# Kernel tuning notes

Hardware: AMD Instinct MI355X
Metric: run time of the kernel (lower is better)

## Reference

```python
import jax, jax.numpy as jnp
import numpy as np

N_NODES = 2048


def setup_inputs() -> dict:
    key = jax.random.key(0)
    ks = jax.random.split(key, 9)
    N, IN, HID, OUT, R, B1 = N_NODES, 64, 32, 16, 4, 1
    s = 0.1
    return {
        "x": jax.random.normal(ks[0], (N, IN), jnp.float32),
        # adj_initial = ones - eye, as in __init__ (learnable parameter)
        "adj_matrix": jnp.ones((N, N), jnp.float32) - jnp.eye(N, dtype=jnp.float32),
        "bases1": jax.random.normal(ks[1], (B1, IN, HID), jnp.float32) * s,
        "coeff1": jax.random.normal(ks[2], (R, B1), jnp.float32) * s,
        "loop_w1": jax.random.normal(ks[3], (IN, HID), jnp.float32) * s,
        "bias1": jnp.zeros((HID,), jnp.float32),
        "bases2": jax.random.normal(ks[4], (R, HID, OUT), jnp.float32) * s,
        "coeff2": jax.random.normal(ks[5], (R, R), jnp.float32) * s,
        "loop_w2": jax.random.normal(ks[6], (HID, OUT), jnp.float32) * s,
        "bias2": jnp.zeros((OUT,), jnp.float32),
        "edge_type": 0,  # ignored by the module (etype is rebuilt as zeros)
    }


def _rel_graph_conv(h, bases, coeff, loop_w, bias, src, dst, n_nodes, act):
    # basis regularizer: W_r = sum_b coeff[r, b] * bases[b]; all edges have etype 0
    W0 = jnp.einsum('b,bio->io', coeff[0], bases)          # [in, out]
    msg = (h @ W0)[src]                                    # [E, out] gather-by-edge
    agg = jax.ops.segment_sum(msg, dst, num_segments=n_nodes)  # scatter-sum
    out = agg + h @ loop_w + bias                          # self-loop + bias
    return act(out)


def reference(x, adj_matrix, bases1, coeff1, loop_w1, bias1,
              bases2, coeff2, loop_w2, bias2, edge_type):
    N = x.shape[0]
    # sigmoid(adj_matrix) > 0 everywhere (sigmoid(0)=0.5 on the diagonal), so
    # torch.nonzero yields ALL N^2 pairs in row-major order: complete graph
    # with self-loops. Structure is static -> build edges with arange.
    idx = jnp.arange(N)
    src = jnp.repeat(idx, N)   # [N*N]
    dst = jnp.tile(idx, N)     # [N*N]
    h = _rel_graph_conv(x, bases1, coeff1, loop_w1, bias1, src, dst, N, jax.nn.relu)
    h = _rel_graph_conv(h, bases2, coeff2, loop_w2, bias2, src, dst, N, lambda z: z)
    return h
```

## Files before the change

### kernel.cpp

```cpp
#include <hip/hip_runtime.h>

#define NN   2048
#define IN   64
#define HID  32
#define OUTD 16

#define S0P 0
#define H1O 4096
#define S1P (4096 + NN * HID)

__global__ __launch_bounds__(256) void k1_colsum_x(const float* __restrict__ x,
                                                   float* __restrict__ ws) {
    __shared__ float red[256];
    const int tid = threadIdx.x, b = blockIdx.x;
    const int col = tid & 63, grp = tid >> 6;
    const float* xb = x + b * 32 * IN;
    float s = 0.f;
#pragma unroll
    for (int r = 0; r < 8; ++r)
        s += xb[(grp * 8 + r) * IN + col];
    red[tid] = s;
    __syncthreads();
    if (tid < 64)
        ws[S0P + b * 64 + tid] = red[tid] + red[tid + 64] + red[tid + 128] + red[tid + 192];
}

__global__ __launch_bounds__(256) void k2_layer1(const float* __restrict__ x,
                                                 const float* __restrict__ bases1,
                                                 const float* __restrict__ coeff1,
                                                 const float* __restrict__ loop_w1,
                                                 const float* __restrict__ bias1,
                                                 float* __restrict__ ws) {
    __shared__ float w1sh[IN * HID];
    __shared__ float xsh[32 * IN];
    __shared__ float s0sh[IN];
    __shared__ float agg1sh[HID];
    __shared__ float red[256];
    const int tid = threadIdx.x, b = blockIdx.x;

    const float4* x4  = (const float4*)(x + b * 32 * IN);
    const float4* w14 = (const float4*)loop_w1;
    float4 xa = x4[tid], xb4 = x4[tid + 256];
    float4 wa = w14[tid], wb = w14[tid + 256];

    {
        const int col = tid & 63, g = tid >> 6;
        float a0 = 0.f, a1 = 0.f, a2 = 0.f, a3 = 0.f;
#pragma unroll
        for (int k = 0; k < 4; ++k) {
            a0 += ws[S0P + (g * 16 + k     ) * 64 + col];
            a1 += ws[S0P + (g * 16 + 4 + k ) * 64 + col];
            a2 += ws[S0P + (g * 16 + 8 + k ) * 64 + col];
            a3 += ws[S0P + (g * 16 + 12 + k) * 64 + col];
        }
        ((float4*)xsh)[tid] = xa; ((float4*)xsh)[tid + 256] = xb4;
        ((float4*)w1sh)[tid] = wa; ((float4*)w1sh)[tid + 256] = wb;
        red[tid] = a0 + a1 + a2 + a3;
    }
    __syncthreads();
    if (tid < 64)
        s0sh[tid] = red[tid] + red[tid + 64] + red[tid + 128] + red[tid + 192];
    __syncthreads();

    {
        const int h = tid & 31, seg = tid >> 5;
        float p = 0.f;
#pragma unroll
        for (int k = 0; k < 8; ++k)
            p += s0sh[seg * 8 + k] * bases1[(seg * 8 + k) * HID + h];
        red[tid] = p;
        __syncthreads();
        if (tid < HID) {
            float t = 0.f;
#pragma unroll
            for (int g = 0; g < 8; ++g) t += red[g * 32 + tid];
            agg1sh[tid] = bias1[tid] + coeff1[0] * t;
        }
    }
    __syncthreads();

    {
        const int h = tid & 31, rgrp = tid >> 5;
        const float agg1v = agg1sh[h];
        float a0 = agg1v, a1 = agg1v, a2 = agg1v, a3 = agg1v;
#pragma unroll
        for (int k = 0; k < IN; ++k) {
            const float w = w1sh[k * HID + h];
            a0 += xsh[(rgrp +  0) * IN + k] * w;
            a1 += xsh[(rgrp +  8) * IN + k] * w;
            a2 += xsh[(rgrp + 16) * IN + k] * w;
            a3 += xsh[(rgrp + 24) * IN + k] * w;
        }
        a0 = fmaxf(a0, 0.f); a1 = fmaxf(a1, 0.f);
        a2 = fmaxf(a2, 0.f); a3 = fmaxf(a3, 0.f);
        float* h1b = ws + H1O + b * 32 * HID;
        h1b[(rgrp +  0) * HID + h] = a0;
        h1b[(rgrp +  8) * HID + h] = a1;
        h1b[(rgrp + 16) * HID + h] = a2;
        h1b[(rgrp + 24) * HID + h] = a3;
        red[tid] = a0 + a1 + a2 + a3;
    }
    __syncthreads();
    if (tid < HID) {
        float t = 0.f;
#pragma unroll
        for (int g = 0; g < 8; ++g) t += red[g * 32 + tid];
        ws[S1P + b * HID + tid] = t;
    }
}

__global__ __launch_bounds__(256) void k3_layer2(const float* __restrict__ bases2,
                                                 const float* __restrict__ coeff2,
                                                 const float* __restrict__ loop_w2,
                                                 const float* __restrict__ bias2,
                                                 const float* __restrict__ ws,
                                                 float* __restrict__ out) {
    __shared__ float w2sh[HID * OUTD];
    __shared__ float w2csh[HID * OUTD];
    __shared__ float h1sh[16 * (HID + 1)];
    __shared__ float s1sh[HID];
    __shared__ float agg2sh[OUTD];
    __shared__ float red[256];
    const int tid = threadIdx.x, b = blockIdx.x;

    {
        const float c20 = coeff2[0], c21 = coeff2[1], c22 = coeff2[2], c23 = coeff2[3];
#pragma unroll
        for (int j = 0; j < 2; ++j) {
            const int i = tid + j * 256;
            w2sh[i]  = loop_w2[i];
            w2csh[i] = c20 * bases2[i]        + c21 * bases2[512 + i] +
                       c22 * bases2[1024 + i] + c23 * bases2[1536 + i];
        }
    }
    for (int j = 0; j < 2; ++j) {
        const int i = tid + j * 256;
        h1sh[(i >> 5) * (HID + 1) + (i & 31)] = ws[H1O + b * 16 * HID + i];
    }
    {
        const int h = tid & 31, g = tid >> 5;
        float a0 = 0.f, a1 = 0.f;
#pragma unroll
        for (int k = 0; k < 4; ++k) {
            a0 += ws[S1P + (g * 8 + k    ) * HID + h];
            a1 += ws[S1P + (g * 8 + 4 + k) * HID + h];
        }
        red[tid] = a0 + a1;
    }
    __syncthreads();
    if (tid < HID) {
        float t = 0.f;
#pragma unroll
        for (int g = 0; g < 8; ++g) t += red[g * 32 + tid];
        s1sh[tid] = t;
    }
    __syncthreads();
    if (tid < OUTD) {
        float s = 0.f;
#pragma unroll
        for (int h = 0; h < HID; ++h) s += s1sh[h] * w2csh[h * OUTD + tid];
        agg2sh[tid] = bias2[tid] + s;
    }
    __syncthreads();

    {
        const int row = tid >> 4, o = tid & 15;
        float acc = agg2sh[o];
#pragma unroll
        for (int h = 0; h < HID; ++h)
            acc += h1sh[row * (HID + 1) + h] * w2sh[h * OUTD + o];
        out[b * 256 + tid] = acc;
    }
}

extern "C" void kernel_launch(void* const* d_in, const int* in_sizes, int n_in,
                              void* d_out, int out_size, void* d_ws, size_t ws_size,
                              hipStream_t stream) {
    const float* x       = (const float*)d_in[0];
    const float* bases1  = (const float*)d_in[2];
    const float* coeff1  = (const float*)d_in[3];
    const float* loop_w1 = (const float*)d_in[4];
    const float* bias1   = (const float*)d_in[5];
    const float* bases2  = (const float*)d_in[6];
    const float* coeff2  = (const float*)d_in[7];
    const float* loop_w2 = (const float*)d_in[8];
    const float* bias2   = (const float*)d_in[9];
    float* out = (float*)d_out;
    float* ws  = (float*)d_ws;

    k1_colsum_x<<<64, 256, 0, stream>>>(x, ws);
    k2_layer1 <<<64, 256, 0, stream>>>(x, bases1, coeff1, loop_w1, bias1, ws);
    k3_layer2 <<<128, 256, 0, stream>>>(bases2, coeff2, loop_w2, bias2, ws, out);
}
```

Measured before the change: 89.29 us.

## Fuse three kernels into one persistent kernel with flag-based grid barriers

Merges the column-sum, layer-1 and layer-2 kernels into a single 64-block launch. Cross-block reductions are synchronised with magic-value release/acquire flags in workspace instead of kernel boundaries. Layer-1 activations stay in shared memory rather than going through global memory. This removes two launch gaps and the h1 global round-trip. In exchange it relies on all 64 blocks being co-resident and on spin barriers with a guard timeout. Flags are never reset, so stale values from a previous call could satisfy the barrier early.

```diff
diff --git a/kernel.cpp b/kernel.cpp
--- a/kernel.cpp
+++ b/kernel.cpp
@@ -4,58 +4,93 @@
 #define IN   64
 #define HID  32
 #define OUTD 16
+#define NB   64
+#define MAGICA 0x5CA1AB1Eu
+#define MAGICB 0x00DDBA11u
 
 #define S0P 0
-#define H1O 4096
-#define S1P (4096 + NN * HID)
-
-__global__ __launch_bounds__(256) void k1_colsum_x(const float* __restrict__ x,
-                                                   float* __restrict__ ws) {
+#define FLA 4096
+#define S1P 4160
+#define FLB 6208
+
+__global__ __launch_bounds__(256) void rgcn_1node(
+    const float* __restrict__ x,
+    const float* __restrict__ bases1,
+    const float* __restrict__ coeff1,
+    const float* __restrict__ loop_w1,
+    const float* __restrict__ bias1,
+    const float* __restrict__ bases2,
+    const float* __restrict__ coeff2,
+    const float* __restrict__ loop_w2,
+    const float* __restrict__ bias2,
+    float* __restrict__ ws,
+    float* __restrict__ out)
+{
+    __shared__ float xsh[32 * IN];
+    __shared__ float w1sh[IN * HID];
+    __shared__ float w2sh[HID * OUTD];
+    __shared__ float w2csh[HID * OUTD];
+    __shared__ float h1sh[32 * (HID + 1)];
     __shared__ float red[256];
-    const int tid = threadIdx.x, b = blockIdx.x;
-    const int col = tid & 63, grp = tid >> 6;
-    const float* xb = x + b * 32 * IN;
-    float s = 0.f;
-#pragma unroll
-    for (int r = 0; r < 8; ++r)
-        s += xb[(grp * 8 + r) * IN + col];
-    red[tid] = s;
-    __syncthreads();
-    if (tid < 64)
-        ws[S0P + b * 64 + tid] = red[tid] + red[tid + 64] + red[tid + 128] + red[tid + 192];
-}
-
-__global__ __launch_bounds__(256) void k2_layer1(const float* __restrict__ x,
-                                                 const float* __restrict__ bases1,
-                                                 const float* __restrict__ coeff1,
-                                                 const float* __restrict__ loop_w1,
-                                                 const float* __restrict__ bias1,
-                                                 float* __restrict__ ws) {
-    __shared__ float w1sh[IN * HID];
-    __shared__ float xsh[32 * IN];
     __shared__ float s0sh[IN];
     __shared__ float agg1sh[HID];
-    __shared__ float red[256];
+    __shared__ float s1sh[HID];
+    __shared__ float agg2sh[OUTD];
+
     const int tid = threadIdx.x, b = blockIdx.x;
+    unsigned int* flagsA = (unsigned int*)ws + FLA;
+    unsigned int* flagsB = (unsigned int*)ws + FLB;
 
     const float4* x4  = (const float4*)(x + b * 32 * IN);
     const float4* w14 = (const float4*)loop_w1;
-    float4 xa = x4[tid], xb4 = x4[tid + 256];
+    float4 xa = x4[tid], xb = x4[tid + 256];
     float4 wa = w14[tid], wb = w14[tid + 256];
+    const float c20 = coeff2[0], c21 = coeff2[1], c22 = coeff2[2], c23 = coeff2[3];
+    float w2v0 = loop_w2[tid], w2v1 = loop_w2[tid + 256];
+    float wc0 = c20 * bases2[tid]       + c21 * bases2[512 + tid] +
+                c22 * bases2[1024 + tid]+ c23 * bases2[1536 + tid];
+    float wc1 = c20 * bases2[256 + tid] + c21 * bases2[768 + tid] +
+                c22 * bases2[1280 + tid]+ c23 * bases2[1792 + tid];
+    ((float4*)xsh)[tid] = xa;  ((float4*)xsh)[tid + 256] = xb;
+    ((float4*)w1sh)[tid] = wa; ((float4*)w1sh)[tid + 256] = wb;
+    w2sh[tid] = w2v0;  w2sh[tid + 256] = w2v1;
+    w2csh[tid] = wc0;  w2csh[tid + 256] = wc1;
+    __syncthreads();
+
+    {
+        const int col = tid & 63, grp = tid >> 6;
+        float s = 0.f;
+#pragma unroll
+        for (int r = 0; r < 8; ++r) s += xsh[(grp * 8 + r) * IN + col];
+        red[tid] = s;
+    }
+    __syncthreads();
+    if (tid < 64) {
+        float v = red[tid] + red[tid + 64] + red[tid + 128] + red[tid + 192];
+        __hip_atomic_store(&ws[S0P + b * 64 + tid], v,
+                           __ATOMIC_RELAXED, __HIP_MEMORY_SCOPE_AGENT);
+    }
+    __syncthreads();
+    if (tid == 0)
+        __hip_atomic_store(&flagsA[b], MAGICA,
+                           __ATOMIC_RELEASE, __HIP_MEMORY_SCOPE_AGENT);
+    if (tid < 64) {
+        int guard = 0; unsigned v;
+        do {
+            v = __hip_atomic_load(&flagsA[tid],
+                                  __ATOMIC_ACQUIRE, __HIP_MEMORY_SCOPE_AGENT);
+        } while (v != MAGICA && ++guard < 4000000);
+    }
+    __syncthreads();
 
     {
         const int col = tid & 63, g = tid >> 6;
-        float a0 = 0.f, a1 = 0.f, a2 = 0.f, a3 = 0.f;
-#pragma unroll
-        for (int k = 0; k < 4; ++k) {
-            a0 += ws[S0P + (g * 16 + k     ) * 64 + col];
-            a1 += ws[S0P + (g * 16 + 4 + k ) * 64 + col];
-            a2 += ws[S0P + (g * 16 + 8 + k ) * 64 + col];
-            a3 += ws[S0P + (g * 16 + 12 + k) * 64 + col];
-        }
-        ((float4*)xsh)[tid] = xa; ((float4*)xsh)[tid + 256] = xb4;
-        ((float4*)w1sh)[tid] = wa; ((float4*)w1sh)[tid + 256] = wb;
-        red[tid] = a0 + a1 + a2 + a3;
+        float s = 0.f;
+#pragma unroll
+        for (int k = 0; k < 16; ++k)
+            s += __hip_atomic_load(&ws[S0P + (g * 16 + k) * 64 + col],
+                                   __ATOMIC_RELAXED, __HIP_MEMORY_SCOPE_AGENT);
+        red[tid] = s;
     }
     __syncthreads();
     if (tid < 64)
@@ -69,20 +104,20 @@
         for (int k = 0; k < 8; ++k)
             p += s0sh[seg * 8 + k] * bases1[(seg * 8 + k) * HID + h];
         red[tid] = p;
-        __syncthreads();
-        if (tid < HID) {
-            float t = 0.f;
-#pragma unroll
-            for (int g = 0; g < 8; ++g) t += red[g * 32 + tid];
-            agg1sh[tid] = bias1[tid] + coeff1[0] * t;
-        }
+    }
+    __syncthreads();
+    if (tid < HID) {
+        float t = 0.f;
+#pragma unroll
+        for (int g = 0; g < 8; ++g) t += red[g * 32 + tid];
+        agg1sh[tid] = bias1[tid] + coeff1[0] * t;
     }
     __syncthreads();
 
     {
         const int h = tid & 31, rgrp = tid >> 5;
-        const float agg1v = agg1sh[h];
-        float a0 = agg1v, a1 = agg1v, a2 = agg1v, a3 = agg1v;
+        const float A = agg1sh[h];
+        float a0 = A, a1 = A, a2 = A, a3 = A;
 #pragma unroll
         for (int k = 0; k < IN; ++k) {
             const float w = w1sh[k * HID + h];
@@ -93,11 +128,10 @@
         }
         a0 = fmaxf(a0, 0.f); a1 = fmaxf(a1, 0.f);
         a2 = fmaxf(a2, 0.f); a3 = fmaxf(a3, 0.f);
-        float* h1b = ws + H1O + b * 32 * HID;
-        h1b[(rgrp +  0) * HID + h] = a0;
-        h1b[(rgrp +  8) * HID + h] = a1;
-        h1b[(rgrp + 16) * HID + h] = a2;
-        h1b[(rgrp + 24) * HID + h] = a3;
+        h1sh[(rgrp +  0) * (HID + 1) + h] = a0;
+        h1sh[(rgrp +  8) * (HID + 1) + h] = a1;
+        h1sh[(rgrp + 16) * (HID + 1) + h] = a2;
+        h1sh[(rgrp + 24) * (HID + 1) + h] = a3;
         red[tid] = a0 + a1 + a2 + a3;
     }
     __syncthreads();
@@ -105,47 +139,30 @@
         float t = 0.f;
 #pragma unroll
         for (int g = 0; g < 8; ++g) t += red[g * 32 + tid];
-        ws[S1P + b * HID + tid] = t;
-    }
-}
-
-__global__ __launch_bounds__(256) void k3_layer2(const float* __restrict__ bases2,
-                                                 const float* __restrict__ coeff2,
-                                                 const float* __restrict__ loop_w2,
-                                                 const float* __restrict__ bias2,
-                                                 const float* __restrict__ ws,
-                                                 float* __restrict__ out) {
-    __shared__ float w2sh[HID * OUTD];
-    __shared__ float w2csh[HID * OUTD];
-    __shared__ float h1sh[16 * (HID + 1)];
-    __shared__ float s1sh[HID];
-    __shared__ float agg2sh[OUTD];
-    __shared__ float red[256];
-    const int tid = threadIdx.x, b = blockIdx.x;
-
-    {
-        const float c20 = coeff2[0], c21 = coeff2[1], c22 = coeff2[2], c23 = coeff2[3];
-#pragma unroll
-        for (int j = 0; j < 2; ++j) {
-            const int i = tid + j * 256;
-            w2sh[i]  = loop_w2[i];
-            w2csh[i] = c20 * bases2[i]        + c21 * bases2[512 + i] +
-                       c22 * bases2[1024 + i] + c23 * bases2[1536 + i];
-        }
-    }
-    for (int j = 0; j < 2; ++j) {
-        const int i = tid + j * 256;
-        h1sh[(i >> 5) * (HID + 1) + (i & 31)] = ws[H1O + b * 16 * HID + i];
-    }
+        __hip_atomic_store(&ws[S1P + b * HID + tid], t,
+                           __ATOMIC_RELAXED, __HIP_MEMORY_SCOPE_AGENT);
+    }
+    __syncthreads();
+    if (tid == 0)
+        __hip_atomic_store(&flagsB[b], MAGICB,
+                           __ATOMIC_RELEASE, __HIP_MEMORY_SCOPE_AGENT);
+    if (tid < 64) {
+        int guard = 0; unsigned v;
+        do {
+            v = __hip_atomic_load(&flagsB[tid],
+                                  __ATOMIC_ACQUIRE, __HIP_MEMORY_SCOPE_AGENT);
+        } while (v != MAGICB && ++guard < 4000000);
+    }
+    __syncthreads();
+
     {
         const int h = tid & 31, g = tid >> 5;
-        float a0 = 0.f, a1 = 0.f;
-#pragma unroll
-        for (int k = 0; k < 4; ++k) {
-            a0 += ws[S1P + (g * 8 + k    ) * HID + h];
-            a1 += ws[S1P + (g * 8 + 4 + k) * HID + h];
-        }
-        red[tid] = a0 + a1;
+        float s = 0.f;
+#pragma unroll
+        for (int k = 0; k < 8; ++k)
+            s += __hip_atomic_load(&ws[S1P + (g * 8 + k) * HID + h],
+                                   __ATOMIC_RELAXED, __HIP_MEMORY_SCOPE_AGENT);
+        red[tid] = s;
     }
     __syncthreads();
     if (tid < HID) {
@@ -163,13 +180,15 @@
     }
     __syncthreads();
 
-    {
-        const int row = tid >> 4, o = tid & 15;
+#pragma unroll
+    for (int j = 0; j < 2; ++j) {
+        const int idx = tid + j * 256;
+        const int row = idx >> 4, o = idx & 15;
         float acc = agg2sh[o];
 #pragma unroll
         for (int h = 0; h < HID; ++h)
             acc += h1sh[row * (HID + 1) + h] * w2sh[h * OUTD + o];
-        out[b * 256 + tid] = acc;
+        out[b * 512 + idx] = acc;
     }
 }
 
@@ -188,7 +207,6 @@
     float* out = (float*)d_out;
     float* ws  = (float*)d_ws;
 
-    k1_colsum_x<<<64, 256, 0, stream>>>(x, ws);
-    k2_layer1 <<<64, 256, 0, stream>>>(x, bases1, coeff1, loop_w1, bias1, ws);
-    k3_layer2 <<<128, 256, 0, stream>>>(bases2, coeff2, loop_w2, bias2, ws, out);
+    rgcn_1node<<<NB, 256, 0, stream>>>(x, bases1, coeff1, loop_w1, bias1,
+                                       bases2, coeff2, loop_w2, bias2, ws, out);
 }
```

After: 93.17 us. +4.3%, slower.

## Fuse x column-sum into layer-1 kernel, each block recomputing the full reduction

Applied to the files above, without the earlier changes.

Removes the separate column-sum kernel. Every layer-1 block now reads all of x (512 KB) itself with float4 loads and reduces it to the 64 column sums, instead of reading per-block partials from workspace. This saves one kernel launch and the global round-trip between kernels. In exchange, the reads of x grow 64-fold in total (mostly served from L2) and each block carries 16 float4 accumulators in registers.

```diff
diff --git a/kernel.cpp b/kernel.cpp
--- a/kernel.cpp
+++ b/kernel.cpp
@@ -5,61 +5,59 @@
 #define HID  32
 #define OUTD 16
 
-#define S0P 0
-#define H1O 4096
-#define S1P (4096 + NN * HID)
+#define H1O 0
+#define S1P (NN * HID)
 
-__global__ __launch_bounds__(256) void k1_colsum_x(const float* __restrict__ x,
-                                                   float* __restrict__ ws) {
-    __shared__ float red[256];
-    const int tid = threadIdx.x, b = blockIdx.x;
-    const int col = tid & 63, grp = tid >> 6;
-    const float* xb = x + b * 32 * IN;
-    float s = 0.f;
-#pragma unroll
-    for (int r = 0; r < 8; ++r)
-        s += xb[(grp * 8 + r) * IN + col];
-    red[tid] = s;
-    __syncthreads();
-    if (tid < 64)
-        ws[S0P + b * 64 + tid] = red[tid] + red[tid + 64] + red[tid + 128] + red[tid + 192];
-}
-
-__global__ __launch_bounds__(256) void k2_layer1(const float* __restrict__ x,
+__global__ __launch_bounds__(256) void kA_layer1(const float* __restrict__ x,
                                                  const float* __restrict__ bases1,
                                                  const float* __restrict__ coeff1,
                                                  const float* __restrict__ loop_w1,
                                                  const float* __restrict__ bias1,
                                                  float* __restrict__ ws) {
+    __shared__ float xsh[32 * IN];
     __shared__ float w1sh[IN * HID];
-    __shared__ float xsh[32 * IN];
+    __shared__ float red4[1024];
     __shared__ float s0sh[IN];
     __shared__ float agg1sh[HID];
     __shared__ float red[256];
     const int tid = threadIdx.x, b = blockIdx.x;
 
-    const float4* x4  = (const float4*)(x + b * 32 * IN);
+    const float4* xt4 = (const float4*)(x + b * 32 * IN);
     const float4* w14 = (const float4*)loop_w1;
-    float4 xa = x4[tid], xb4 = x4[tid + 256];
+    float4 xa = xt4[tid], xb = xt4[tid + 256];
     float4 wa = w14[tid], wb = w14[tid + 256];
 
     {
-        const int col = tid & 63, g = tid >> 6;
-        float a0 = 0.f, a1 = 0.f, a2 = 0.f, a3 = 0.f;
+        const float4* x4 = (const float4*)x;
+        float4 acc[16];
 #pragma unroll
-        for (int k = 0; k < 4; ++k) {
-            a0 += ws[S0P + (g * 16 + k     ) * 64 + col];
-            a1 += ws[S0P + (g * 16 + 4 + k ) * 64 + col];
-            a2 += ws[S0P + (g * 16 + 8 + k ) * 64 + col];
-            a3 += ws[S0P + (g * 16 + 12 + k) * 64 + col];
+        for (int k = 0; k < 16; ++k) acc[k] = make_float4(0.f, 0.f, 0.f, 0.f);
+#pragma unroll
+        for (int ol = 0; ol < 8; ++ol) {
+#pragma unroll
+            for (int k = 0; k < 16; ++k) {
+                const float4 v = x4[ol * 4096 + k * 256 + tid];
+                acc[k].x += v.x; acc[k].y += v.y; acc[k].z += v.z; acc[k].w += v.w;
+            }
         }
-        ((float4*)xsh)[tid] = xa; ((float4*)xsh)[tid + 256] = xb4;
+#pragma unroll
+        for (int k = 1; k < 16; ++k) {
+            acc[0].x += acc[k].x; acc[0].y += acc[k].y;
+            acc[0].z += acc[k].z; acc[0].w += acc[k].w;
+        }
+        ((float4*)red4)[tid] = acc[0];
+        ((float4*)xsh)[tid] = xa;  ((float4*)xsh)[tid + 256] = xb;
         ((float4*)w1sh)[tid] = wa; ((float4*)w1sh)[tid + 256] = wb;
-        red[tid] = a0 + a1 + a2 + a3;
     }
     __syncthreads();
-    if (tid < 64)
-        s0sh[tid] = red[tid] + red[tid + 64] + red[tid + 128] + red[tid + 192];
+    if (tid < IN) {
+        const int cg = tid >> 2, comp = tid & 3;
+        float s = 0.f;
+#pragma unroll
+        for (int j = 0; j < 16; ++j)
+            s += red4[(cg + 16 * j) * 4 + comp];
+        s0sh[tid] = s;
+    }
     __syncthreads();
 
     {
@@ -69,20 +67,20 @@
         for (int k = 0; k < 8; ++k)
             p += s0sh[seg * 8 + k] * bases1[(seg * 8 + k) * HID + h];
         red[tid] = p;
-        __syncthreads();
-        if (tid < HID) {
-            float t = 0.f;
+    }
+    __syncthreads();
+    if (tid < HID) {
+        float t = 0.f;
 #pragma unroll
-            for (int g = 0; g < 8; ++g) t += red[g * 32 + tid];
-            agg1sh[tid] = bias1[tid] + coeff1[0] * t;
-        }
+        for (int g = 0; g < 8; ++g) t += red[g * 32 + tid];
+        agg1sh[tid] = bias1[tid] + coeff1[0] * t;
     }
     __syncthreads();
 
     {
         const int h = tid & 31, rgrp = tid >> 5;
-        const float agg1v = agg1sh[h];
-        float a0 = agg1v, a1 = agg1v, a2 = agg1v, a3 = agg1v;
+        const float A = agg1sh[h];
+        float a0 = A, a1 = A, a2 = A, a3 = A;
 #pragma unroll
         for (int k = 0; k < IN; ++k) {
             const float w = w1sh[k * HID + h];
@@ -109,7 +107,7 @@
     }
 }
 
-__global__ __launch_bounds__(256) void k3_layer2(const float* __restrict__ bases2,
+__global__ __launch_bounds__(256) void kB_layer2(const float* __restrict__ bases2,
                                                  const float* __restrict__ coeff2,
                                                  const float* __restrict__ loop_w2,
                                                  const float* __restrict__ bias2,
@@ -133,6 +131,7 @@
                        c22 * bases2[1024 + i] + c23 * bases2[1536 + i];
         }
     }
+#pragma unroll
     for (int j = 0; j < 2; ++j) {
         const int i = tid + j * 256;
         h1sh[(i >> 5) * (HID + 1) + (i & 31)] = ws[H1O + b * 16 * HID + i];
@@ -162,7 +161,6 @@
         agg2sh[tid] = bias2[tid] + s;
     }
     __syncthreads();
-
     {
         const int row = tid >> 4, o = tid & 15;
         float acc = agg2sh[o];
@@ -188,7 +186,6 @@
     float* out = (float*)d_out;
     float* ws  = (float*)d_ws;
 
-    k1_colsum_x<<<64, 256, 0, stream>>>(x, ws);
-    k2_layer1 <<<64, 256, 0, stream>>>(x, bases1, coeff1, loop_w1, bias1, ws);
-    k3_layer2 <<<128, 256, 0, stream>>>(bases2, coeff2, loop_w2, bias2, ws, out);
+    kA_layer1<<<64, 256, 0, stream>>>(x, bases1, coeff1, loop_w1, bias1, ws);
+    kB_layer2<<<128, 256, 0, stream>>>(bases2, coeff2, loop_w2, bias2, ws, out);
 }
```

Result: slower. 99.40 us (+11.3%).

## Restructure into two kernels with transposed pre-activation and redundant per-block colsum

Applied to the files above, without the earlier changes.

Merges the three-kernel pipeline into two launches. The first kernel computes the column sums of x and the pre-bias product x@loop_w1, storing the latter transposed. The second kernel has every block redundantly rebuild agg1, apply relu and sum h1 over all nodes itself, then compute layer 2 for its 32 rows. This removes one launch and one global dependency step. In exchange each block rereads the whole 256 KB transposed buffer and repeats the reduction.

```diff
diff --git a/kernel.cpp b/kernel.cpp
--- a/kernel.cpp
+++ b/kernel.cpp
@@ -6,56 +6,98 @@
 #define OUTD 16
 
 #define S0P 0
-#define H1O 4096
-#define S1P (4096 + NN * HID)
+#define ZT  4096
 
-__global__ __launch_bounds__(256) void k1_colsum_x(const float* __restrict__ x,
-                                                   float* __restrict__ ws) {
+__global__ __launch_bounds__(256) void kA_z_s0(const float* __restrict__ x,
+                                               const float* __restrict__ loop_w1,
+                                               float* __restrict__ ws) {
+    __shared__ float xsh[32 * IN];
+    __shared__ float w1sh[IN * HID];
+    __shared__ float zsh[32 * 33];
     __shared__ float red[256];
     const int tid = threadIdx.x, b = blockIdx.x;
-    const int col = tid & 63, grp = tid >> 6;
-    const float* xb = x + b * 32 * IN;
-    float s = 0.f;
+
+    const float4* xt4 = (const float4*)(x + b * 32 * IN);
+    const float4* w14 = (const float4*)loop_w1;
+    float4 xa = xt4[tid], xb = xt4[tid + 256];
+    float4 wa = w14[tid], wb = w14[tid + 256];
+    ((float4*)xsh)[tid] = xa;  ((float4*)xsh)[tid + 256] = xb;
+    ((float4*)w1sh)[tid] = wa; ((float4*)w1sh)[tid + 256] = wb;
+    __syncthreads();
+
+    {
+        const int col = tid & 63, grp = tid >> 6;
+        float s = 0.f;
 #pragma unroll
-    for (int r = 0; r < 8; ++r)
-        s += xb[(grp * 8 + r) * IN + col];
-    red[tid] = s;
+        for (int r = 0; r < 8; ++r) s += xsh[(grp * 8 + r) * IN + col];
+        red[tid] = s;
+    }
     __syncthreads();
     if (tid < 64)
         ws[S0P + b * 64 + tid] = red[tid] + red[tid + 64] + red[tid + 128] + red[tid + 192];
+
+    {
+        const int h = tid & 31, rgrp = tid >> 5;
+        float a0 = 0.f, a1 = 0.f, a2 = 0.f, a3 = 0.f;
+#pragma unroll
+        for (int k = 0; k < IN; ++k) {
+            const float w = w1sh[k * HID + h];
+            a0 += xsh[(rgrp +  0) * IN + k] * w;
+            a1 += xsh[(rgrp +  8) * IN + k] * w;
+            a2 += xsh[(rgrp + 16) * IN + k] * w;
+            a3 += xsh[(rgrp + 24) * IN + k] * w;
+        }
+        zsh[(rgrp +  0) * 33 + h] = a0;
+        zsh[(rgrp +  8) * 33 + h] = a1;
+        zsh[(rgrp + 16) * 33 + h] = a2;
+        zsh[(rgrp + 24) * 33 + h] = a3;
+    }
+    __syncthreads();
+
+#pragma unroll
+    for (int j = 0; j < 4; ++j) {
+        const int i = tid + 256 * j;
+        const int hh = i >> 5, rr = i & 31;
+        ws[ZT + hh * NN + b * 32 + rr] = zsh[rr * 33 + hh];
+    }
 }
 
-__global__ __launch_bounds__(256) void k2_layer1(const float* __restrict__ x,
-                                                 const float* __restrict__ bases1,
-                                                 const float* __restrict__ coeff1,
-                                                 const float* __restrict__ loop_w1,
-                                                 const float* __restrict__ bias1,
-                                                 float* __restrict__ ws) {
-    __shared__ float w1sh[IN * HID];
-    __shared__ float xsh[32 * IN];
+__global__ __launch_bounds__(256) void kB_rest(const float* __restrict__ bases1,
+                                               const float* __restrict__ coeff1,
+                                               const float* __restrict__ bias1,
+                                               const float* __restrict__ bases2,
+                                               const float* __restrict__ coeff2,
+                                               const float* __restrict__ loop_w2,
+                                               const float* __restrict__ bias2,
+                                               const float* __restrict__ ws,
+                                               float* __restrict__ out) {
+    __shared__ float w2sh[HID * OUTD];
+    __shared__ float w2csh[HID * OUTD];
+    __shared__ float h1own[32 * 33];
+    __shared__ float red[256];
     __shared__ float s0sh[IN];
     __shared__ float agg1sh[HID];
-    __shared__ float red[256];
+    __shared__ float s1sh[HID];
+    __shared__ float agg2sh[OUTD];
     const int tid = threadIdx.x, b = blockIdx.x;
 
-    const float4* x4  = (const float4*)(x + b * 32 * IN);
-    const float4* w14 = (const float4*)loop_w1;
-    float4 xa = x4[tid], xb4 = x4[tid + 256];
-    float4 wa = w14[tid], wb = w14[tid + 256];
-
+    {
+        const float c20 = coeff2[0], c21 = coeff2[1], c22 = coeff2[2], c23 = coeff2[3];
+#pragma unroll
+        for (int j = 0; j < 2; ++j) {
+            const int i = tid + j * 256;
+            w2sh[i]  = loop_w2[i];
+            w2csh[i] = c20 * bases2[i]        + c21 * bases2[512 + i] +
+                       c22 * bases2[1024 + i] + c23 * bases2[1536 + i];
+        }
+    }
     {
         const int col = tid & 63, g = tid >> 6;
-        float a0 = 0.f, a1 = 0.f, a2 = 0.f, a3 = 0.f;
+        float s = 0.f;
 #pragma unroll
-        for (int k = 0; k < 4; ++k) {
-            a0 += ws[S0P + (g * 16 + k     ) * 64 + col];
-            a1 += ws[S0P + (g * 16 + 4 + k ) * 64 + col];
-            a2 += ws[S0P + (g * 16 + 8 + k ) * 64 + col];
-            a3 += ws[S0P + (g * 16 + 12 + k) * 64 + col];
-        }
-        ((float4*)xsh)[tid] = xa; ((float4*)xsh)[tid + 256] = xb4;
-        ((float4*)w1sh)[tid] = wa; ((float4*)w1sh)[tid + 256] = wb;
-        red[tid] = a0 + a1 + a2 + a3;
+        for (int k = 0; k < 16; ++k)
+            s += ws[S0P + (g * 16 + k) * 64 + col];
+        red[tid] = s;
     }
     __syncthreads();
     if (tid < 64)
@@ -69,89 +111,37 @@
         for (int k = 0; k < 8; ++k)
             p += s0sh[seg * 8 + k] * bases1[(seg * 8 + k) * HID + h];
         red[tid] = p;
-        __syncthreads();
-        if (tid < HID) {
-            float t = 0.f;
-#pragma unroll
-            for (int g = 0; g < 8; ++g) t += red[g * 32 + tid];
-            agg1sh[tid] = bias1[tid] + coeff1[0] * t;
-        }
-    }
-    __syncthreads();
-
-    {
-        const int h = tid & 31, rgrp = tid >> 5;
-        const float agg1v = agg1sh[h];
-        float a0 = agg1v, a1 = agg1v, a2 = agg1v, a3 = agg1v;
-#pragma unroll
-        for (int k = 0; k < IN; ++k) {
-            const float w = w1sh[k * HID + h];
-            a0 += xsh[(rgrp +  0) * IN + k] * w;
-            a1 += xsh[(rgrp +  8) * IN + k] * w;
-            a2 += xsh[(rgrp + 16) * IN + k] * w;
-            a3 += xsh[(rgrp + 24) * IN + k] * w;
-        }
-        a0 = fmaxf(a0, 0.f); a1 = fmaxf(a1, 0.f);
-        a2 = fmaxf(a2, 0.f); a3 = fmaxf(a3, 0.f);
-        float* h1b = ws + H1O + b * 32 * HID;
-        h1b[(rgrp +  0) * HID + h] = a0;
-        h1b[(rgrp +  8) * HID + h] = a1;
-        h1b[(rgrp + 16) * HID + h] = a2;
-        h1b[(rgrp + 24) * HID + h] = a3;
-        red[tid] = a0 + a1 + a2 + a3;
     }
     __syncthreads();
     if (tid < HID) {
         float t = 0.f;
 #pragma unroll
         for (int g = 0; g < 8; ++g) t += red[g * 32 + tid];
-        ws[S1P + b * HID + tid] = t;
+        agg1sh[tid] = bias1[tid] + coeff1[0] * t;
     }
-}
-
-__global__ __launch_bounds__(256) void k3_layer2(const float* __restrict__ bases2,
-                                                 const float* __restrict__ coeff2,
-                                                 const float* __restrict__ loop_w2,
-                                                 const float* __restrict__ bias2,
-                                                 const float* __restrict__ ws,
-                                                 float* __restrict__ out) {
-    __shared__ float w2sh[HID * OUTD];
-    __shared__ float w2csh[HID * OUTD];
-    __shared__ float h1sh[16 * (HID + 1)];
-    __shared__ float s1sh[HID];
-    __shared__ float agg2sh[OUTD];
-    __shared__ float red[256];
-    const int tid = threadIdx.x, b = blockIdx.x;
+    __syncthreads();
 
     {
-        const float c20 = coeff2[0], c21 = coeff2[1], c22 = coeff2[2], c23 = coeff2[3];
-#pragma unroll
-        for (int j = 0; j < 2; ++j) {
-            const int i = tid + j * 256;
-            w2sh[i]  = loop_w2[i];
-            w2csh[i] = c20 * bases2[i]        + c21 * bases2[512 + i] +
-                       c22 * bases2[1024 + i] + c23 * bases2[1536 + i];
+        const int h = tid >> 3, sub = tid & 7;
+        const float a1h = agg1sh[h];
+        const float4* z4 = (const float4*)(ws + ZT);
+        float4 acc = make_float4(0.f, 0.f, 0.f, 0.f);
+#pragma unroll 8
+        for (int j = 0; j < 64; ++j) {
+            const int jj = (j + b) & 63;
+            const float4 v = z4[h * (NN / 4) + 8 * jj + sub];
+            acc.x += fmaxf(v.x + a1h, 0.f);
+            acc.y += fmaxf(v.y + a1h, 0.f);
+            acc.z += fmaxf(v.z + a1h, 0.f);
+            acc.w += fmaxf(v.w + a1h, 0.f);
         }
-    }
-    for (int j = 0; j < 2; ++j) {
-        const int i = tid + j * 256;
-        h1sh[(i >> 5) * (HID + 1) + (i & 31)] = ws[H1O + b * 16 * HID + i];
-    }
-    {
-        const int h = tid & 31, g = tid >> 5;
-        float a0 = 0.f, a1 = 0.f;
-#pragma unroll
-        for (int k = 0; k < 4; ++k) {
-            a0 += ws[S1P + (g * 8 + k    ) * HID + h];
-            a1 += ws[S1P + (g * 8 + 4 + k) * HID + h];
-        }
-        red[tid] = a0 + a1;
+        red[tid] = acc.x + acc.y + acc.z + acc.w;
     }
     __syncthreads();
     if (tid < HID) {
         float t = 0.f;
 #pragma unroll
-        for (int g = 0; g < 8; ++g) t += red[g * 32 + tid];
+        for (int k = 0; k < 8; ++k) t += red[tid * 8 + k];
         s1sh[tid] = t;
     }
     __syncthreads();
@@ -161,15 +151,23 @@
         for (int h = 0; h < HID; ++h) s += s1sh[h] * w2csh[h * OUTD + tid];
         agg2sh[tid] = bias2[tid] + s;
     }
+#pragma unroll
+    for (int j = 0; j < 4; ++j) {
+        const int i = tid + 256 * j;
+        const int hh = i >> 5, rr = i & 31;
+        h1own[rr * 33 + hh] = fmaxf(ws[ZT + hh * NN + b * 32 + rr] + agg1sh[hh], 0.f);
+    }
     __syncthreads();
 
-    {
-        const int row = tid >> 4, o = tid & 15;
+#pragma unroll
+    for (int j = 0; j < 2; ++j) {
+        const int idx = tid + j * 256;
+        const int row = idx >> 4, o = idx & 15;
         float acc = agg2sh[o];
 #pragma unroll
         for (int h = 0; h < HID; ++h)
-            acc += h1sh[row * (HID + 1) + h] * w2sh[h * OUTD + o];
-        out[b * 256 + tid] = acc;
+            acc += h1own[row * 33 + h] * w2sh[h * OUTD + o];
+        out[b * 512 + idx] = acc;
     }
 }
 
@@ -188,7 +186,7 @@
     float* out = (float*)d_out;
     float* ws  = (float*)d_ws;
 
-    k1_colsum_x<<<64, 256, 0, stream>>>(x, ws);
-    k2_layer1 <<<64, 256, 0, stream>>>(x, bases1, coeff1, loop_w1, bias1, ws);
-    k3_layer2 <<<128, 256, 0, stream>>>(bases2, coeff2, loop_w2, bias2, ws, out);
+    kA_z_s0<<<64, 256, 0, stream>>>(x, loop_w1, ws);
+    kB_rest<<<64, 256, 0, stream>>>(bases1, coeff1, bias1,
+                                    bases2, coeff2, loop_w2, bias2, ws, out);
 }
```

Result: no change. 90.46 us (+1.3%).
